# Kernel optimization log

Measured on AMD Instinct MI355X. Metric: run time of the kernel, lower is better.

## Reference

```python
import jax, jax.numpy as jnp
import numpy as np
import math

D_MODEL = 1024
N_HEADS = 16
D_HEAD = 64
NEG = 1e10


def setup_inputs() -> dict:
    key = jax.random.key(0)
    k0, k1, k2, k3, k4 = jax.random.split(key, 5)
    B, T = 4, 2048
    x = jax.random.normal(k0, (B, T, D_MODEL), dtype=jnp.float32)
    s = 0.02
    W_Q = jax.random.normal(k1, (D_MODEL, N_HEADS * D_HEAD), dtype=jnp.float32) * s
    W_K = jax.random.normal(k2, (D_MODEL, N_HEADS * D_HEAD), dtype=jnp.float32) * s
    W_V = jax.random.normal(k3, (D_MODEL, N_HEADS * D_HEAD), dtype=jnp.float32) * s
    W_O = jax.random.normal(k4, (N_HEADS * D_HEAD, D_MODEL), dtype=jnp.float32) * s
    return {"x": x, "W_Q": W_Q, "W_K": W_K, "W_V": W_V, "W_O": W_O}


def reference(x, W_Q, W_K, W_V, W_O):
    B, T, _ = x.shape
    # project and split heads: [B, nh, T, dh]
    def heads(t):
        return t.reshape(B, T, N_HEADS, D_HEAD).transpose(0, 2, 1, 3)
    q = heads(x @ W_Q)
    k = heads(x @ W_K)
    v = heads(x @ W_V)
    scores = jnp.einsum('bhqd,bhkd->bhqk', q, k)  # [B, nh, T, T]
    # faithful to source: tril(scores) - 1e10 * (1 - tril_mask), THEN divide by sqrt(d_head)
    mask = jnp.tril(jnp.ones((T, T), dtype=scores.dtype))
    masked = scores * mask - NEG * (1.0 - mask)
    attn = jax.nn.softmax(masked / math.sqrt(D_HEAD), axis=-1)
    z = jnp.einsum('bhqk,bhkd->bhqd', attn, v)
    z_flat = z.transpose(0, 2, 1, 3).reshape(B, T, N_HEADS * D_HEAD)
    return z_flat @ W_O
```

## Files before the change

### kernel.cpp

```cpp
#include <hip/hip_runtime.h>
#include <cstdint>
#include <cstddef>

#define DEV __device__ __forceinline__

typedef __attribute__((ext_vector_type(8))) short short8;
typedef __attribute__((ext_vector_type(8))) unsigned short ushort8;
typedef __attribute__((ext_vector_type(4))) unsigned short ushortx4;
typedef __attribute__((ext_vector_type(4))) float floatx4;


DEV unsigned short f2bf(float f) {
    union { float f; uint32_t u; } v; v.f = f;
    uint32_t r = v.u + 0x7FFFu + ((v.u >> 16) & 1u);
    return (unsigned short)(r >> 16);
}

DEV void gld16(const void* g, void* l) {
    __builtin_amdgcn_global_load_lds(
        (const __attribute__((address_space(1))) unsigned int*)g,
        (__attribute__((address_space(3))) unsigned int*)l, 16, 0, 0);
}

template<int NIT>
DEV void stage_swz(const unsigned short* g, int ld, unsigned short* lds) {
    int t = threadIdx.x;
#pragma unroll
    for (int i = 0; i < NIT; ++i) {
        int idx = i * 256 + t;
        int r   = idx >> 3;
        int cl  = idx & 7;
        int cs  = cl ^ (r & 7);
        gld16(g + (size_t)r * ld + cs * 8, lds + idx * 8);
    }
}

DEV short8 ld_frag(const unsigned short* lds, int row, int chunk) {
    int c = chunk ^ (row & 7);
    return *(const short8*)(lds + row * 64 + c * 8);
}


__global__ void cvt_x_kernel(const float* __restrict__ x, unsigned short* __restrict__ xb) {
    int i = (blockIdx.x * 256 + threadIdx.x) * 4;
    floatx4 v = *(const floatx4*)(x + i);
    ushortx4 o = { f2bf(v[0]), f2bf(v[1]), f2bf(v[2]), f2bf(v[3]) };
    *(ushortx4*)(xb + i) = o;
}


__global__ void trans_w_kernel(const float* __restrict__ W0, const float* __restrict__ W1,
                               const float* __restrict__ W2, const float* __restrict__ W3,
                               unsigned short* __restrict__ T0, unsigned short* __restrict__ T1,
                               unsigned short* __restrict__ T2, unsigned short* __restrict__ T3) {
    const float* W = (blockIdx.z == 0) ? W0 : (blockIdx.z == 1) ? W1 : (blockIdx.z == 2) ? W2 : W3;
    unsigned short* T = (blockIdx.z == 0) ? T0 : (blockIdx.z == 1) ? T1 : (blockIdx.z == 2) ? T2 : T3;
    __shared__ float tile[32][33];
    int kb = blockIdx.x * 32, nb = blockIdx.y * 32;
    int tx = threadIdx.x & 31, ty = threadIdx.x >> 5;
#pragma unroll
    for (int i = 0; i < 4; ++i)
        tile[ty + i * 8][tx] = W[(size_t)(kb + ty + i * 8) * 1024 + nb + tx];
    __syncthreads();
#pragma unroll
    for (int i = 0; i < 4; ++i)
        T[(size_t)(nb + ty + i * 8) * 1024 + kb + tx] = f2bf(tile[tx][ty + i * 8]);
}


template<int MODE>
__global__ __launch_bounds__(256, 2) void gemm_kernel(
    const unsigned short* __restrict__ A,
    const unsigned short* __restrict__ B0, const unsigned short* __restrict__ B1,
    const unsigned short* __restrict__ B2,
    unsigned short* __restrict__ oq, unsigned short* __restrict__ ok,
    unsigned short* __restrict__ ov, float* __restrict__ of) {
    __shared__ __align__(16) unsigned short Ab[128 * 64];
    __shared__ __align__(16) unsigned short Bb[128 * 64];
    const int bx = blockIdx.x, by = blockIdx.y, bz = blockIdx.z;
    const unsigned short* Bt = (MODE == 0) ? (bz == 0 ? B0 : (bz == 1 ? B1 : B2)) : B0;
    const int l = threadIdx.x & 63, w = threadIdx.x >> 6;
    const int l16 = l & 15, l4 = l >> 4;
    const int wr = w >> 1, wc = w & 1;
    const int m0 = by * 128, n0 = bx * 128;

    floatx4 acc[4][4];
#pragma unroll
    for (int i = 0; i < 4; ++i)
#pragma unroll
        for (int j = 0; j < 4; ++j) acc[i][j] = (floatx4){0.f, 0.f, 0.f, 0.f};

    const unsigned short* Ag = A + (size_t)m0 * 1024;
    const unsigned short* Bg = Bt + (size_t)n0 * 1024;

    for (int kt = 0; kt < 16; ++kt) {
        __syncthreads();
        stage_swz<4>(Ag + kt * 64, 1024, Ab);
        stage_swz<4>(Bg + kt * 64, 1024, Bb);
        __syncthreads();

        short8 af[4][2], bfr[4][2];
#pragma unroll
        for (int mi = 0; mi < 4; ++mi) {
            int row = wr * 64 + mi * 16 + l16;
#pragma unroll
            for (int kc = 0; kc < 2; ++kc) af[mi][kc] = ld_frag(Ab, row, kc * 4 + l4);
        }
#pragma unroll
        for (int ni = 0; ni < 4; ++ni) {
            int row = wc * 64 + ni * 16 + l16;
#pragma unroll
            for (int kc = 0; kc < 2; ++kc) bfr[ni][kc] = ld_frag(Bb, row, kc * 4 + l4);
        }
#pragma unroll
        for (int mi = 0; mi < 4; ++mi)
#pragma unroll
            for (int ni = 0; ni < 4; ++ni) {
                acc[mi][ni] = __builtin_amdgcn_mfma_f32_16x16x32_bf16(af[mi][0], bfr[ni][0], acc[mi][ni], 0, 0, 0);
                acc[mi][ni] = __builtin_amdgcn_mfma_f32_16x16x32_bf16(af[mi][1], bfr[ni][1], acc[mi][ni], 0, 0, 0);
            }
    }

    if (MODE == 0) {
        unsigned short* dst = (bz == 0) ? oq : (bz == 1) ? ok : ov;
#pragma unroll
        for (int mi = 0; mi < 4; ++mi)
#pragma unroll
            for (int ni = 0; ni < 4; ++ni)
#pragma unroll
                for (int r = 0; r < 4; ++r) {
                    int mm = m0 + wr * 64 + mi * 16 + l4 * 4 + r;
                    int nn = n0 + wc * 64 + ni * 16 + l16;
                    int b = mm >> 11, t = mm & 2047, h = nn >> 6, d = nn & 63;
                    dst[(((size_t)(b * 16 + h)) * 2048 + t) * 64 + d] = f2bf(acc[mi][ni][r]);
                }
    } else {
#pragma unroll
        for (int mi = 0; mi < 4; ++mi)
#pragma unroll
            for (int ni = 0; ni < 4; ++ni)
#pragma unroll
                for (int r = 0; r < 4; ++r) {
                    int mm = m0 + wr * 64 + mi * 16 + l4 * 4 + r;
                    int nn = n0 + wc * 64 + ni * 16 + l16;
                    of[(size_t)mm * 1024 + nn] = acc[mi][ni][r];
                }
    }
}


DEV void qk_softmax(const short8 kf0[4], const short8 kf1[4], const short8 qf[2],
                    short8& pb0, short8& pb1, float& sl,
                    bool diag, int w, int l16, int l4) {
    floatx4 st[4];
#pragma unroll
    for (int ki = 0; ki < 4; ++ki) {
        floatx4 z4 = (floatx4){0.f, 0.f, 0.f, 0.f};
        z4 = __builtin_amdgcn_mfma_f32_16x16x32_bf16(kf0[ki], qf[0], z4, 0, 0, 0);
        z4 = __builtin_amdgcn_mfma_f32_16x16x32_bf16(kf1[ki], qf[1], z4, 0, 0, 0);
        st[ki] = z4;
    }

    float p[4][4];
    float psum = 0.f;
#pragma unroll
    for (int ki = 0; ki < 4; ++ki)
#pragma unroll
        for (int r = 0; r < 4; ++r) {
            float val = st[ki][r] * 0.125f;
            if (diag && (ki * 16 + l4 * 4 + r) > (w * 16 + l16)) val = -1.25e9f;
            float e = __expf(val);
            p[ki][r] = e;
            psum += e;
        }
    psum += __shfl_xor(psum, 16);
    psum += __shfl_xor(psum, 32);
    sl += psum;

    short8 t0, t1;
#pragma unroll
    for (int r = 0; r < 4; ++r) {
        t0[r]     = (short)f2bf(p[0][r]);
        t0[4 + r] = (short)f2bf(p[1][r]);
        t1[r]     = (short)f2bf(p[2][r]);
        t1[4 + r] = (short)f2bf(p[3][r]);
    }
    pb0 = t0; pb1 = t1;
}

__global__ __launch_bounds__(256, 2) void attn_kernel(
    const unsigned short* __restrict__ Q, const unsigned short* __restrict__ K,
    const unsigned short* __restrict__ V, unsigned short* __restrict__ Z) {
    __shared__ __align__(16) unsigned short Klds[2][64 * 64];
    __shared__ __align__(16) unsigned short Vlds[2][64 * 72];

    const int bh = blockIdx.x;
    const int j  = blockIdx.y;
    const int qta = j, qtb = 31 - j;
    const int l = threadIdx.x & 63, w = threadIdx.x >> 6;
    const int l16 = l & 15, l4 = l >> 4;

    const unsigned short* Qg = Q + (size_t)bh * 2048 * 64;
    const unsigned short* Kg = K + (size_t)bh * 2048 * 64;
    const unsigned short* Vg = V + (size_t)bh * 2048 * 64;

    const int kl = (l & 35) | ((l & 12) << 1) | ((l & 16) >> 2);

    short8 qfa[2], qfb[2];
    {
        const unsigned short* qrow = Qg + (size_t)(qta * 64 + w * 16 + l16) * 64;
        qfa[0] = *(const short8*)(qrow + l4 * 8);
        qfa[1] = *(const short8*)(qrow + 32 + l4 * 8);
        qrow = Qg + (size_t)(qtb * 64 + w * 16 + l16) * 64;
        qfb[0] = *(const short8*)(qrow + l4 * 8);
        qfb[1] = *(const short8*)(qrow + 32 + l4 * 8);
    }

    floatx4 oa[4], ob[4];
    float sla = 0.f, slb = 0.f;
#pragma unroll
    for (int i = 0; i < 4; ++i) {
        oa[i] = (floatx4){0.f, 0.f, 0.f, 0.f};
        ob[i] = (floatx4){0.f, 0.f, 0.f, 0.f};
    }

    stage_swz<2>(Kg, 64, Klds[0]);
    {
        const unsigned short* vrow = Vg + (size_t)l * 64 + w * 16;
        ushort8 v0 = *(const ushort8*)(vrow);
        ushort8 v1 = *(const ushort8*)(vrow + 8);
#pragma unroll
        for (int jj = 0; jj < 8; ++jj) Vlds[0][(w * 16 + jj) * 72 + kl] = v0[jj];
#pragma unroll
        for (int jj = 0; jj < 8; ++jj) Vlds[0][(w * 16 + 8 + jj) * 72 + kl] = v1[jj];
    }
    __syncthreads();

    for (int kt = 0; kt <= qtb; ++kt) {
        const int cur = kt & 1;
        const bool pf = kt < qtb;
        ushort8 v0, v1;
        if (pf) {
            stage_swz<2>(Kg + (size_t)(kt + 1) * 64 * 64, 64, Klds[cur ^ 1]);
            const unsigned short* vrow = Vg + (size_t)((kt + 1) * 64 + l) * 64 + w * 16;
            v0 = *(const ushort8*)(vrow);
            v1 = *(const ushort8*)(vrow + 8);
        }

        short8 kf0[4], kf1[4];
#pragma unroll
        for (int ki = 0; ki < 4; ++ki) {
            int row = ki * 16 + l16;
            kf0[ki] = ld_frag(Klds[cur], row, l4);
            kf1[ki] = ld_frag(Klds[cur], row, 4 + l4);
        }

        short8 pbb0, pbb1, pba0, pba1;
        qk_softmax(kf0, kf1, qfb, pbb0, pbb1, slb, kt == qtb, w, l16, l4);
        const bool doA = kt <= qta;
        if (doA)
            qk_softmax(kf0, kf1, qfa, pba0, pba1, sla, kt == qta, w, l16, l4);

        const unsigned short* Vl = Vlds[cur];
#pragma unroll
        for (int di = 0; di < 4; ++di) {
            int vr = di * 16 + l16;
            short8 bv0 = *(const short8*)(Vl + vr * 72 + l4 * 8);
            short8 bv1 = *(const short8*)(Vl + vr * 72 + 32 + l4 * 8);
            ob[di] = __builtin_amdgcn_mfma_f32_16x16x32_bf16(bv0, pbb0, ob[di], 0, 0, 0);
            ob[di] = __builtin_amdgcn_mfma_f32_16x16x32_bf16(bv1, pbb1, ob[di], 0, 0, 0);
            if (doA) {
                oa[di] = __builtin_amdgcn_mfma_f32_16x16x32_bf16(bv0, pba0, oa[di], 0, 0, 0);
                oa[di] = __builtin_amdgcn_mfma_f32_16x16x32_bf16(bv1, pba1, oa[di], 0, 0, 0);
            }
        }

        if (pf) {
            unsigned short* Vn = Vlds[cur ^ 1];
#pragma unroll
            for (int jj = 0; jj < 8; ++jj) Vn[(w * 16 + jj) * 72 + kl] = v0[jj];
#pragma unroll
            for (int jj = 0; jj < 8; ++jj) Vn[(w * 16 + 8 + jj) * 72 + kl] = v1[jj];
        }
        __syncthreads();
    }

    const int b = bh >> 4;
    const int hh = (bh & 15) * 64;
    {
        float inv = 1.f / sla;
        unsigned short* zp = Z + ((size_t)b * 2048 + qta * 64 + w * 16 + l16) * 1024 + hh;
#pragma unroll
        for (int di = 0; di < 4; ++di)
#pragma unroll
            for (int r = 0; r < 4; ++r)
                zp[di * 16 + l4 * 4 + r] = f2bf(oa[di][r] * inv);
    }
    {
        float inv = 1.f / slb;
        unsigned short* zp = Z + ((size_t)b * 2048 + qtb * 64 + w * 16 + l16) * 1024 + hh;
#pragma unroll
        for (int di = 0; di < 4; ++di)
#pragma unroll
            for (int r = 0; r < 4; ++r)
                zp[di * 16 + l4 * 4 + r] = f2bf(ob[di][r] * inv);
    }
}


extern "C" void kernel_launch(void* const* d_in, const int* in_sizes, int n_in,
                              void* d_out, int out_size, void* d_ws, size_t ws_size,
                              hipStream_t stream) {
    const float* x  = (const float*)d_in[0];
    const float* WQ = (const float*)d_in[1];
    const float* WK = (const float*)d_in[2];
    const float* WV = (const float*)d_in[3];
    const float* WO = (const float*)d_in[4];
    float* out = (float*)d_out;

    char* ws = (char*)d_ws;
    const size_t MB = 1024 * 1024;
    unsigned short* xb  = (unsigned short*)(ws);
    unsigned short* wqt = (unsigned short*)(ws + 16 * MB);
    unsigned short* wkt = (unsigned short*)(ws + 18 * MB);
    unsigned short* wvt = (unsigned short*)(ws + 20 * MB);
    unsigned short* wot = (unsigned short*)(ws + 22 * MB);
    unsigned short* qb  = (unsigned short*)(ws + 24 * MB);
    unsigned short* kb  = (unsigned short*)(ws + 40 * MB);
    unsigned short* vb  = (unsigned short*)(ws + 56 * MB);
    unsigned short* zb  = xb;

    cvt_x_kernel<<<8192, 256, 0, stream>>>(x, xb);
    trans_w_kernel<<<dim3(32, 32, 4), 256, 0, stream>>>(WQ, WK, WV, WO, wqt, wkt, wvt, wot);
    gemm_kernel<0><<<dim3(8, 64, 3), 256, 0, stream>>>(xb, wqt, wkt, wvt, qb, kb, vb, nullptr);
    attn_kernel<<<dim3(64, 16), 256, 0, stream>>>(qb, kb, vb, zb);
    gemm_kernel<1><<<dim3(8, 64, 1), 256, 0, stream>>>(zb, wot, nullptr, nullptr,
                                                       nullptr, nullptr, nullptr, out);
}
```

Measured before the change: 259.2 us.

## Use HIP bf16 conversion, exp2 softmax, and swizzled GEMM block order

Replaces the hand-written float-to-bf16 rounding with the HIP library intrinsic, which may lower to a hardware conversion instruction. The softmax now folds log2(e) into the scale and calls exp2f instead of __expf. The GEMM block index is also remapped so that consecutive blocks share B columns, aiming for better L2 reuse. Library NaN handling may differ slightly, and the remap assumes an 8x64 grid.

```diff
diff --git a/kernel.cpp b/kernel.cpp
--- a/kernel.cpp
+++ b/kernel.cpp
@@ -1,4 +1,5 @@
 #include <hip/hip_runtime.h>
+#include <hip/hip_bf16.h>
 #include <cstdint>
 #include <cstddef>
 
@@ -10,10 +11,10 @@
 typedef __attribute__((ext_vector_type(4))) float floatx4;
 
 
-DEV unsigned short f2bf(float f) {
-    union { float f; uint32_t u; } v; v.f = f;
-    uint32_t r = v.u + 0x7FFFu + ((v.u >> 16) & 1u);
-    return (unsigned short)(r >> 16);
+DEV unsigned short bfc(float f) {
+    union { __hip_bfloat16 b; unsigned short u; } c;
+    c.b = __float2bfloat16(f);
+    return c.u;
 }
 
 DEV void gld16(const void* g, void* l) {
@@ -44,7 +45,7 @@
 __global__ void cvt_x_kernel(const float* __restrict__ x, unsigned short* __restrict__ xb) {
     int i = (blockIdx.x * 256 + threadIdx.x) * 4;
     floatx4 v = *(const floatx4*)(x + i);
-    ushortx4 o = { f2bf(v[0]), f2bf(v[1]), f2bf(v[2]), f2bf(v[3]) };
+    ushortx4 o = { bfc(v[0]), bfc(v[1]), bfc(v[2]), bfc(v[3]) };
     *(ushortx4*)(xb + i) = o;
 }
 
@@ -64,7 +65,7 @@
     __syncthreads();
 #pragma unroll
     for (int i = 0; i < 4; ++i)
-        T[(size_t)(nb + ty + i * 8) * 1024 + kb + tx] = f2bf(tile[tx][ty + i * 8]);
+        T[(size_t)(nb + ty + i * 8) * 1024 + kb + tx] = bfc(tile[tx][ty + i * 8]);
 }
 
 
@@ -77,7 +78,10 @@
     unsigned short* __restrict__ ov, float* __restrict__ of) {
     __shared__ __align__(16) unsigned short Ab[128 * 64];
     __shared__ __align__(16) unsigned short Bb[128 * 64];
-    const int bx = blockIdx.x, by = blockIdx.y, bz = blockIdx.z;
+    const int bz = blockIdx.z;
+    const int lin = blockIdx.x + 8 * blockIdx.y;
+    const int bx  = (lin >> 3) & 7;
+    const int by  = (lin & 7) * 8 + (lin >> 6);
     const unsigned short* Bt = (MODE == 0) ? (bz == 0 ? B0 : (bz == 1 ? B1 : B2)) : B0;
     const int l = threadIdx.x & 63, w = threadIdx.x >> 6;
     const int l16 = l & 15, l4 = l >> 4;
@@ -132,7 +136,7 @@
                     int mm = m0 + wr * 64 + mi * 16 + l4 * 4 + r;
                     int nn = n0 + wc * 64 + ni * 16 + l16;
                     int b = mm >> 11, t = mm & 2047, h = nn >> 6, d = nn & 63;
-                    dst[(((size_t)(b * 16 + h)) * 2048 + t) * 64 + d] = f2bf(acc[mi][ni][r]);
+                    dst[(((size_t)(b * 16 + h)) * 2048 + t) * 64 + d] = bfc(acc[mi][ni][r]);
                 }
     } else {
 #pragma unroll
@@ -149,6 +153,8 @@
 }
 
 
+#define SCL2 0.18033688011112042f
+
 DEV void qk_softmax(const short8 kf0[4], const short8 kf1[4], const short8 qf[2],
                     short8& pb0, short8& pb1, float& sl,
                     bool diag, int w, int l16, int l4) {
@@ -167,9 +173,9 @@
     for (int ki = 0; ki < 4; ++ki)
 #pragma unroll
         for (int r = 0; r < 4; ++r) {
-            float val = st[ki][r] * 0.125f;
-            if (diag && (ki * 16 + l4 * 4 + r) > (w * 16 + l16)) val = -1.25e9f;
-            float e = __expf(val);
+            float val = st[ki][r] * SCL2;
+            if (diag && (ki * 16 + l4 * 4 + r) > (w * 16 + l16)) val = -1e9f;
+            float e = exp2f(val);
             p[ki][r] = e;
             psum += e;
         }
@@ -180,10 +186,10 @@
     short8 t0, t1;
 #pragma unroll
     for (int r = 0; r < 4; ++r) {
-        t0[r]     = (short)f2bf(p[0][r]);
-        t0[4 + r] = (short)f2bf(p[1][r]);
-        t1[r]     = (short)f2bf(p[2][r]);
-        t1[4 + r] = (short)f2bf(p[3][r]);
+        t0[r]     = (short)bfc(p[0][r]);
+        t0[4 + r] = (short)bfc(p[1][r]);
+        t1[r]     = (short)bfc(p[2][r]);
+        t1[4 + r] = (short)bfc(p[3][r]);
     }
     pb0 = t0; pb1 = t1;
 }
@@ -294,7 +300,7 @@
         for (int di = 0; di < 4; ++di)
 #pragma unroll
             for (int r = 0; r < 4; ++r)
-                zp[di * 16 + l4 * 4 + r] = f2bf(oa[di][r] * inv);
+                zp[di * 16 + l4 * 4 + r] = bfc(oa[di][r] * inv);
     }
     {
         float inv = 1.f / slb;
@@ -303,7 +309,7 @@
         for (int di = 0; di < 4; ++di)
 #pragma unroll
             for (int r = 0; r < 4; ++r)
-                zp[di * 16 + l4 * 4 + r] = f2bf(ob[di][r] * inv);
+                zp[di * 16 + l4 * 4 + r] = bfc(ob[di][r] * inv);
     }
 }
 
```

Result: slower. 267.4 us (+3.1%).
